# Kernel optimization log

Hardware: AMD Instinct MI355X
Metric: run time of the kernel (lower is better)

Reference implementation:

```python
import jax, jax.numpy as jnp
import numpy as np

B, S, DIN, DOUT = 2, 2048, 4096, 4096


def setup_inputs() -> dict:
    key = jax.random.key(0)
    k1, k2 = jax.random.split(key)
    x = jax.random.normal(k1, (B, S, DIN), dtype=jnp.float32)
    weight = jax.random.normal(k2, (DOUT, DIN), dtype=jnp.float32) * 0.02
    # xnor init for row scaling pattern
    mean = weight.mean(-1, keepdims=True)                      # [DOUT,1]
    scale = jnp.abs(weight - mean).mean(-1, keepdims=True)     # [DOUT,1]
    wscale = scale
    wbias = mean
    return {"x": x, "weight": weight, "wscale": wscale, "wbias": wbias}


def reference(x, weight, wscale, wbias):
    # STE binarization: forward = sign(weight) (grad handled in bwd module)
    w_bin = jnp.sign(weight)
    w = wscale * w_bin + wbias                                 # [DOUT, DIN]
    # F.linear(x, w): x @ w.T, no bias
    out = jnp.einsum('bsk,nk->bsn', x, w)
    return out
```

## Files before the change

kernel.cpp:

```cpp
#include <hip/hip_runtime.h>
#include <stdint.h>


#define MDIM 4096
#define NDIM 4096
#define KDIM 4096

typedef int int4v  __attribute__((ext_vector_type(4)));
typedef int int16v __attribute__((ext_vector_type(16)));

__device__ __forceinline__ int pack4_rn(float a, float b, float c, float d, float inv) {
  int ia = __float2int_rn(a * inv) & 0xff;
  int ib = __float2int_rn(b * inv) & 0xff;
  int ic = __float2int_rn(c * inv) & 0xff;
  int id = __float2int_rn(d * inv) & 0xff;
  return ia | (ib << 8) | (ic << 16) | (id << 24);
}

__device__ __forceinline__ int sgn8(float v) {
  return (v > 0.f) ? 1 : ((v < 0.f) ? 0xff : 0);
}

__global__ __launch_bounds__(256) void prep_kernel(
    const float* __restrict__ x, const float* __restrict__ w,
    char* __restrict__ xq, char* __restrict__ wsg,
    float* __restrict__ xscale, float* __restrict__ sumx) {
  const int b = blockIdx.x;
  const int tid = threadIdx.x;
  if (b < MDIM) {
    const int row = b;
    const float4* xr = (const float4*)(x + (size_t)row * KDIM);
    float4 v[4];
    float s = 0.f, amax = 0.f;
#pragma unroll
    for (int u = 0; u < 4; ++u) {
      v[u] = xr[u * 256 + tid];
      s += v[u].x + v[u].y + v[u].z + v[u].w;
      amax = fmaxf(amax, fmaxf(fmaxf(fabsf(v[u].x), fabsf(v[u].y)),
                               fmaxf(fabsf(v[u].z), fabsf(v[u].w))));
    }
#pragma unroll
    for (int off = 32; off > 0; off >>= 1) {
      s += __shfl_down(s, off, 64);
      amax = fmaxf(amax, __shfl_down(amax, off, 64));
    }
    __shared__ float rs[4], rm[4], bcast;
    if ((tid & 63) == 0) { rs[tid >> 6] = s; rm[tid >> 6] = amax; }
    __syncthreads();
    if (tid == 0) {
      sumx[row] = rs[0] + rs[1] + rs[2] + rs[3];
      float mt = fmaxf(fmaxf(rm[0], rm[1]), fmaxf(rm[2], rm[3]));
      xscale[row] = mt * (1.f / 127.f);
      bcast = (mt > 0.f) ? 127.f / mt : 0.f;
    }
    __syncthreads();
    const float inv = bcast;
    int* xo = (int*)(xq + (size_t)row * KDIM);
#pragma unroll
    for (int u = 0; u < 4; ++u)
      xo[u * 256 + tid] = pack4_rn(v[u].x, v[u].y, v[u].z, v[u].w, inv);
  } else {
    const size_t base = (size_t)(b - MDIM) * (256 * 4);
    const float4* wr = (const float4*)w;
    int* wo = (int*)wsg;
#pragma unroll
    for (int u = 0; u < 4; ++u) {
      size_t i = base + u * 256 + tid;
      float4 v = wr[i];
      wo[i] = sgn8(v.x) | (sgn8(v.y) << 8) | (sgn8(v.z) << 16) | (sgn8(v.w) << 24);
    }
  }
}

__global__ __launch_bounds__(512, 2) void gemm_bin_i8_pipe(
    const char* __restrict__ A, const char* __restrict__ Bs,
    const float* __restrict__ wscale, const float* __restrict__ wbias,
    const float* __restrict__ xscale, const float* __restrict__ sumx,
    float* __restrict__ C) {
  __shared__ __align__(16) char sm[131072];

  const int bm = blockIdx.x >> 4, bn = blockIdx.x & 15;
  const int tm0 = bm * 256, tn0 = bn * 256;
  const int tid = threadIdx.x;
  const int lane = tid & 63, wave = tid >> 6;
  const int col32 = lane & 31, hl = lane >> 5;
  const int wr = wave >> 2, wc = wave & 3;

  int16v acc[4][2];
#pragma unroll
  for (int mi = 0; mi < 4; ++mi)
#pragma unroll
    for (int nj = 0; nj < 2; ++nj)
#pragma unroll
      for (int r = 0; r < 16; ++r) acc[mi][nj][r] = 0;

  int4v afA[4], bqA[2], afB[4], bqB[2];

  int aOff[2][4], bOff[2][2];
#pragma unroll
  for (int ks2 = 0; ks2 < 2; ++ks2) {
#pragma unroll
    for (int mi = 0; mi < 4; ++mi) {
      int row = wr * 128 + mi * 32 + col32;
      int sw = (row >> 1) & 3;
      aOff[ks2][mi] = row * 64 + (((ks2 * 2 + hl) ^ sw) & 3) * 16;
    }
#pragma unroll
    for (int nj = 0; nj < 2; ++nj) {
      int row = wc * 64 + nj * 32 + col32;
      int sw = (row >> 1) & 3;
      bOff[ks2][nj] = 65536 + row * 64 + (((ks2 * 2 + hl) ^ sw) & 3) * 16;
    }
  }

  const int u0 = tid, u1 = tid + 512;
  const int r0 = u0 >> 2, r1 = u1 >> 2;
  const int c0 = (u0 & 3) ^ ((r0 >> 1) & 3);
  const int c1 = (u1 & 3) ^ ((r1 >> 1) & 3);
  const char* gA0 = A + (size_t)(tm0 + r0) * KDIM + c0 * 16;
  const char* gA1 = A + (size_t)(tm0 + r1) * KDIM + c1 * 16;
  const char* gB0 = Bs + (size_t)(tn0 + r0) * KDIM + c0 * 16;
  const char* gB1 = Bs + (size_t)(tn0 + r1) * KDIM + c1 * 16;
  const int ldsu0 = tid * 16, ldsu1 = 8192 + tid * 16;

#define STAGE_A(BUF, KH, KOFS)                                                    \
  do {                                                                            \
    const int base_ = ((BUF) * 2 + (KH)) * 16384;                                 \
    __builtin_amdgcn_global_load_lds(                                             \
        (const __attribute__((address_space(1))) void*)(gA0 + (KOFS)),            \
        (__attribute__((address_space(3))) void*)(sm + base_ + ldsu0), 16, 0, 0); \
    __builtin_amdgcn_global_load_lds(                                             \
        (const __attribute__((address_space(1))) void*)(gA1 + (KOFS)),            \
        (__attribute__((address_space(3))) void*)(sm + base_ + ldsu1), 16, 0, 0); \
  } while (0)

#define STAGE_B(BUF, KH, KOFS)                                                    \
  do {                                                                            \
    const int base_ = 65536 + ((BUF) * 2 + (KH)) * 16384;                         \
    __builtin_amdgcn_global_load_lds(                                             \
        (const __attribute__((address_space(1))) void*)(gB0 + (KOFS)),            \
        (__attribute__((address_space(3))) void*)(sm + base_ + ldsu0), 16, 0, 0); \
    __builtin_amdgcn_global_load_lds(                                             \
        (const __attribute__((address_space(1))) void*)(gB1 + (KOFS)),            \
        (__attribute__((address_space(3))) void*)(sm + base_ + ldsu1), 16, 0, 0); \
  } while (0)

#define DSRD(SET, BUF, KS, KS2)                                                   \
  do {                                                                            \
    _Pragma("unroll") for (int mi_ = 0; mi_ < 4; ++mi_)                           \
        af##SET[mi_] =                                                            \
            *(const int4v*)(sm + ((BUF) * 2 + (KS)) * 16384 + aOff[KS2][mi_]);    \
    _Pragma("unroll") for (int nj_ = 0; nj_ < 2; ++nj_)                           \
        bq##SET[nj_] =                                                            \
            *(const int4v*)(sm + ((BUF) * 2 + (KS)) * 16384 + bOff[KS2][nj_]);    \
  } while (0)

#define MFMA8(SET)                                                                \
  do {                                                                            \
    __builtin_amdgcn_s_setprio(1);                                                \
    _Pragma("unroll") for (int mi_ = 0; mi_ < 4; ++mi_)                           \
        _Pragma("unroll") for (int nj_ = 0; nj_ < 2; ++nj_)                       \
            acc[mi_][nj_] = __builtin_amdgcn_mfma_i32_32x32x32_i8(                \
                af##SET[mi_], bq##SET[nj_], acc[mi_][nj_], 0, 0, 0);              \
    __builtin_amdgcn_s_setprio(0);                                                \
  } while (0)

#define WAITL6                                                                    \
  do {                                                                            \
    asm volatile("s_waitcnt lgkmcnt(6)" ::: "memory");                            \
    __builtin_amdgcn_sched_barrier(0);                                            \
  } while (0)
#define WAITL0                                                                    \
  do {                                                                            \
    asm volatile("s_waitcnt lgkmcnt(0)" ::: "memory");                            \
    __builtin_amdgcn_sched_barrier(0);                                            \
  } while (0)

#define BARO __builtin_amdgcn_s_barrier()
#define CK6  asm volatile("s_waitcnt vmcnt(6)\n\ts_barrier" ::: "memory")
#define CK4  asm volatile("s_waitcnt vmcnt(4)\n\ts_barrier" ::: "memory")
#define CK0  asm volatile("s_waitcnt vmcnt(0)\n\ts_barrier" ::: "memory")

#define PHASEP(CSET, NSET, NBUF, NKS, NKS2, STAGEOP, ENDSYNC)                     \
  do {                                                                            \
    DSRD(NSET, NBUF, NKS, NKS2);                                                  \
    STAGEOP;                                                                      \
    WAITL6;                                                                       \
    MFMA8(CSET);                                                                  \
    ENDSYNC;                                                                      \
  } while (0)

#define TILE_MAIN(BUF, TAU)                                                       \
  do {                                                                            \
    PHASEP(A, B, BUF, 0, 1, STAGE_A((BUF) ^ 1, 1, ((TAU) + 1) * 128 + 64), BARO); \
    PHASEP(B, A, BUF, 1, 0, STAGE_B((BUF) ^ 1, 1, ((TAU) + 1) * 128 + 64), BARO); \
    PHASEP(A, B, BUF, 1, 1, STAGE_A(BUF, 0, ((TAU) + 2) * 128), CK6);             \
    PHASEP(B, A, (BUF) ^ 1, 0, 0, STAGE_B(BUF, 0, ((TAU) + 2) * 128), CK4);       \
  } while (0)

  STAGE_A(0, 0, 0);
  STAGE_B(0, 0, 0);
  STAGE_A(0, 1, 64);
  STAGE_B(0, 1, 64);
  STAGE_A(1, 0, 128);
  STAGE_B(1, 0, 128);
  CK4;
  DSRD(A, 0, 0, 0);

#pragma unroll 1
  for (int t = 0; t < 30; t += 2) {
    TILE_MAIN(0, t);
    TILE_MAIN(1, t + 1);
  }

  PHASEP(A, B, 0, 0, 1, STAGE_A(1, 1, 31 * 128 + 64), BARO);
  PHASEP(B, A, 0, 1, 0, STAGE_B(1, 1, 31 * 128 + 64), BARO);
  PHASEP(A, B, 0, 1, 1, (void)0, CK4);
  PHASEP(B, A, 1, 0, 0, (void)0, CK0);
  PHASEP(A, B, 1, 0, 1, (void)0, BARO);
  PHASEP(B, A, 1, 1, 0, (void)0, BARO);
  PHASEP(A, B, 1, 1, 1, (void)0, BARO);
  WAITL0;
  MFMA8(B);

#undef TILE_MAIN
#undef PHASEP
#undef BARO
#undef CK6
#undef CK4
#undef CK0
#undef WAITL6
#undef WAITL0
#undef MFMA8
#undef DSRD
#undef STAGE_A
#undef STAGE_B

  float wsv[2], wbv[2];
#pragma unroll
  for (int nj = 0; nj < 2; ++nj) {
    int n = tn0 + wc * 64 + nj * 32 + col32;
    wsv[nj] = wscale[n];
    wbv[nj] = wbias[n];
  }
#pragma unroll
  for (int mi = 0; mi < 4; ++mi) {
#pragma unroll
    for (int reg = 0; reg < 16; ++reg) {
      int m = tm0 + wr * 128 + mi * 32 + (reg & 3) + 8 * (reg >> 2) + 4 * hl;
      float xs = xscale[m];
      float sx = sumx[m];
      float* crow = C + (size_t)m * NDIM + tn0 + wc * 64 + col32;
#pragma unroll
      for (int nj = 0; nj < 2; ++nj)
        crow[nj * 32] = wsv[nj] * xs * (float)acc[mi][nj][reg] + wbv[nj] * sx;
    }
  }
}

extern "C" void kernel_launch(void* const* d_in, const int* in_sizes, int n_in,
                              void* d_out, int out_size, void* d_ws, size_t ws_size,
                              hipStream_t stream) {
  const float* x      = (const float*)d_in[0];
  const float* weight = (const float*)d_in[1];
  const float* wscale = (const float*)d_in[2];
  const float* wbias  = (const float*)d_in[3];
  float* out = (float*)d_out;

  char* xq  = (char*)d_ws;
  char* wsg = xq + (size_t)MDIM * KDIM;
  float* xscale = (float*)(wsg + (size_t)NDIM * KDIM);
  float* sumx   = xscale + MDIM;

  prep_kernel<<<MDIM + (NDIM * KDIM) / (16 * 256), 256, 0, stream>>>(
      x, weight, xq, wsg, xscale, sumx);
  gemm_bin_i8_pipe<<<(MDIM / 256) * (NDIM / 256), 512, 0, stream>>>(
      xq, wsg, wscale, wbias, xscale, sumx, out);
}
```

Measured before the change: 234.1 us.

## Use 4 waves per block with 128x128 per-wave tiles in int8 GEMM

Changes the GEMM block from 8 waves (each computing 128x64) to 4 waves, each computing 128x128 with 16 MFMAs per phase, keeping the 256x256 block tile and LDS layout. Each thread now issues 4 global-to-LDS loads per stage, so the vmcnt/lgkmcnt wait thresholds are raised to match. The intent is to cut LDS read traffic per MFMA and barrier overhead, at the cost of more accumulator registers (256 VGPRs of accumulators), fewer waves to hide latency, and one block per CU.

```diff
diff --git a/kernel.cpp b/kernel.cpp
--- a/kernel.cpp
+++ b/kernel.cpp
@@ -72,7 +72,7 @@
   }
 }
 
-__global__ __launch_bounds__(512, 2) void gemm_bin_i8_pipe(
+__global__ __launch_bounds__(256, 1) void gemm_bin_i8_w4(
     const char* __restrict__ A, const char* __restrict__ Bs,
     const float* __restrict__ wscale, const float* __restrict__ wbias,
     const float* __restrict__ xscale, const float* __restrict__ sumx,
@@ -84,19 +84,19 @@
   const int tid = threadIdx.x;
   const int lane = tid & 63, wave = tid >> 6;
   const int col32 = lane & 31, hl = lane >> 5;
-  const int wr = wave >> 2, wc = wave & 3;
-
-  int16v acc[4][2];
+  const int wr = wave >> 1, wc = wave & 1;
+
+  int16v acc[4][4];
 #pragma unroll
   for (int mi = 0; mi < 4; ++mi)
 #pragma unroll
-    for (int nj = 0; nj < 2; ++nj)
+    for (int nj = 0; nj < 4; ++nj)
 #pragma unroll
       for (int r = 0; r < 16; ++r) acc[mi][nj][r] = 0;
 
-  int4v afA[4], bqA[2], afB[4], bqB[2];
-
-  int aOff[2][4], bOff[2][2];
+  int4v afA[4], bqA[4], afB[4], bqB[4];
+
+  int aOff[2][4], bOff[2][4];
 #pragma unroll
   for (int ks2 = 0; ks2 < 2; ++ks2) {
 #pragma unroll
@@ -106,43 +106,43 @@
       aOff[ks2][mi] = row * 64 + (((ks2 * 2 + hl) ^ sw) & 3) * 16;
     }
 #pragma unroll
-    for (int nj = 0; nj < 2; ++nj) {
-      int row = wc * 64 + nj * 32 + col32;
+    for (int nj = 0; nj < 4; ++nj) {
+      int row = wc * 128 + nj * 32 + col32;
       int sw = (row >> 1) & 3;
       bOff[ks2][nj] = 65536 + row * 64 + (((ks2 * 2 + hl) ^ sw) & 3) * 16;
     }
   }
 
-  const int u0 = tid, u1 = tid + 512;
-  const int r0 = u0 >> 2, r1 = u1 >> 2;
-  const int c0 = (u0 & 3) ^ ((r0 >> 1) & 3);
-  const int c1 = (u1 & 3) ^ ((r1 >> 1) & 3);
-  const char* gA0 = A + (size_t)(tm0 + r0) * KDIM + c0 * 16;
-  const char* gA1 = A + (size_t)(tm0 + r1) * KDIM + c1 * 16;
-  const char* gB0 = Bs + (size_t)(tn0 + r0) * KDIM + c0 * 16;
-  const char* gB1 = Bs + (size_t)(tn0 + r1) * KDIM + c1 * 16;
-  const int ldsu0 = tid * 16, ldsu1 = 8192 + tid * 16;
+  const char* gAp[4];
+  const char* gBp[4];
+  int ldq[4];
+#pragma unroll
+  for (int q = 0; q < 4; ++q) {
+    int rowq = (tid >> 2) + 64 * q;
+    int cq = (tid & 3) ^ ((rowq >> 1) & 3);
+    gAp[q] = A + (size_t)(tm0 + rowq) * KDIM + cq * 16;
+    gBp[q] = Bs + (size_t)(tn0 + rowq) * KDIM + cq * 16;
+    ldq[q] = q * 4096 + tid * 16;
+  }
 
 #define STAGE_A(BUF, KH, KOFS)                                                    \
   do {                                                                            \
     const int base_ = ((BUF) * 2 + (KH)) * 16384;                                 \
-    __builtin_amdgcn_global_load_lds(                                             \
-        (const __attribute__((address_space(1))) void*)(gA0 + (KOFS)),            \
-        (__attribute__((address_space(3))) void*)(sm + base_ + ldsu0), 16, 0, 0); \
-    __builtin_amdgcn_global_load_lds(                                             \
-        (const __attribute__((address_space(1))) void*)(gA1 + (KOFS)),            \
-        (__attribute__((address_space(3))) void*)(sm + base_ + ldsu1), 16, 0, 0); \
+    _Pragma("unroll") for (int q_ = 0; q_ < 4; ++q_)                              \
+        __builtin_amdgcn_global_load_lds(                                         \
+            (const __attribute__((address_space(1))) void*)(gAp[q_] + (KOFS)),    \
+            (__attribute__((address_space(3))) void*)(sm + base_ + ldq[q_]),      \
+            16, 0, 0);                                                            \
   } while (0)
 
 #define STAGE_B(BUF, KH, KOFS)                                                    \
   do {                                                                            \
     const int base_ = 65536 + ((BUF) * 2 + (KH)) * 16384;                         \
-    __builtin_amdgcn_global_load_lds(                                             \
-        (const __attribute__((address_space(1))) void*)(gB0 + (KOFS)),            \
-        (__attribute__((address_space(3))) void*)(sm + base_ + ldsu0), 16, 0, 0); \
-    __builtin_amdgcn_global_load_lds(                                             \
-        (const __attribute__((address_space(1))) void*)(gB1 + (KOFS)),            \
-        (__attribute__((address_space(3))) void*)(sm + base_ + ldsu1), 16, 0, 0); \
+    _Pragma("unroll") for (int q_ = 0; q_ < 4; ++q_)                              \
+        __builtin_amdgcn_global_load_lds(                                         \
+            (const __attribute__((address_space(1))) void*)(gBp[q_] + (KOFS)),    \
+            (__attribute__((address_space(3))) void*)(sm + base_ + ldq[q_]),      \
+            16, 0, 0);                                                            \
   } while (0)
 
 #define DSRD(SET, BUF, KS, KS2)                                                   \
@@ -150,24 +150,24 @@
     _Pragma("unroll") for (int mi_ = 0; mi_ < 4; ++mi_)                           \
         af##SET[mi_] =                                                            \
             *(const int4v*)(sm + ((BUF) * 2 + (KS)) * 16384 + aOff[KS2][mi_]);    \
-    _Pragma("unroll") for (int nj_ = 0; nj_ < 2; ++nj_)                           \
+    _Pragma("unroll") for (int nj_ = 0; nj_ < 4; ++nj_)                           \
         bq##SET[nj_] =                                                            \
             *(const int4v*)(sm + ((BUF) * 2 + (KS)) * 16384 + bOff[KS2][nj_]);    \
   } while (0)
 
-#define MFMA8(SET)                                                                \
+#define MFMA16(SET)                                                               \
   do {                                                                            \
     __builtin_amdgcn_s_setprio(1);                                                \
     _Pragma("unroll") for (int mi_ = 0; mi_ < 4; ++mi_)                           \
-        _Pragma("unroll") for (int nj_ = 0; nj_ < 2; ++nj_)                       \
+        _Pragma("unroll") for (int nj_ = 0; nj_ < 4; ++nj_)                       \
             acc[mi_][nj_] = __builtin_amdgcn_mfma_i32_32x32x32_i8(                \
                 af##SET[mi_], bq##SET[nj_], acc[mi_][nj_], 0, 0, 0);              \
     __builtin_amdgcn_s_setprio(0);                                                \
   } while (0)
 
-#define WAITL6                                                                    \
-  do {                                                                            \
-    asm volatile("s_waitcnt lgkmcnt(6)" ::: "memory");                            \
+#define WAITL8                                                                    \
+  do {                                                                            \
+    asm volatile("s_waitcnt lgkmcnt(8)" ::: "memory");                            \
     __builtin_amdgcn_sched_barrier(0);                                            \
   } while (0)
 #define WAITL0                                                                    \
@@ -177,16 +177,16 @@
   } while (0)
 
 #define BARO __builtin_amdgcn_s_barrier()
-#define CK6  asm volatile("s_waitcnt vmcnt(6)\n\ts_barrier" ::: "memory")
-#define CK4  asm volatile("s_waitcnt vmcnt(4)\n\ts_barrier" ::: "memory")
+#define CK12 asm volatile("s_waitcnt vmcnt(12)\n\ts_barrier" ::: "memory")
+#define CK8  asm volatile("s_waitcnt vmcnt(8)\n\ts_barrier" ::: "memory")
 #define CK0  asm volatile("s_waitcnt vmcnt(0)\n\ts_barrier" ::: "memory")
 
 #define PHASEP(CSET, NSET, NBUF, NKS, NKS2, STAGEOP, ENDSYNC)                     \
   do {                                                                            \
     DSRD(NSET, NBUF, NKS, NKS2);                                                  \
     STAGEOP;                                                                      \
-    WAITL6;                                                                       \
-    MFMA8(CSET);                                                                  \
+    WAITL8;                                                                       \
+    MFMA16(CSET);                                                                 \
     ENDSYNC;                                                                      \
   } while (0)
 
@@ -194,8 +194,8 @@
   do {                                                                            \
     PHASEP(A, B, BUF, 0, 1, STAGE_A((BUF) ^ 1, 1, ((TAU) + 1) * 128 + 64), BARO); \
     PHASEP(B, A, BUF, 1, 0, STAGE_B((BUF) ^ 1, 1, ((TAU) + 1) * 128 + 64), BARO); \
-    PHASEP(A, B, BUF, 1, 1, STAGE_A(BUF, 0, ((TAU) + 2) * 128), CK6);             \
-    PHASEP(B, A, (BUF) ^ 1, 0, 0, STAGE_B(BUF, 0, ((TAU) + 2) * 128), CK4);       \
+    PHASEP(A, B, BUF, 1, 1, STAGE_A(BUF, 0, ((TAU) + 2) * 128), CK12);            \
+    PHASEP(B, A, (BUF) ^ 1, 0, 0, STAGE_B(BUF, 0, ((TAU) + 2) * 128), CK8);       \
   } while (0)
 
   STAGE_A(0, 0, 0);
@@ -204,7 +204,7 @@
   STAGE_B(0, 1, 64);
   STAGE_A(1, 0, 128);
   STAGE_B(1, 0, 128);
-  CK4;
+  CK8;
   DSRD(A, 0, 0, 0);
 
 #pragma unroll 1
@@ -215,31 +215,31 @@
 
   PHASEP(A, B, 0, 0, 1, STAGE_A(1, 1, 31 * 128 + 64), BARO);
   PHASEP(B, A, 0, 1, 0, STAGE_B(1, 1, 31 * 128 + 64), BARO);
-  PHASEP(A, B, 0, 1, 1, (void)0, CK4);
+  PHASEP(A, B, 0, 1, 1, (void)0, CK8);
   PHASEP(B, A, 1, 0, 0, (void)0, CK0);
   PHASEP(A, B, 1, 0, 1, (void)0, BARO);
   PHASEP(B, A, 1, 1, 0, (void)0, BARO);
   PHASEP(A, B, 1, 1, 1, (void)0, BARO);
   WAITL0;
-  MFMA8(B);
+  MFMA16(B);
 
 #undef TILE_MAIN
 #undef PHASEP
 #undef BARO
-#undef CK6
-#undef CK4
+#undef CK12
+#undef CK8
 #undef CK0
-#undef WAITL6
+#undef WAITL8
 #undef WAITL0
-#undef MFMA8
+#undef MFMA16
 #undef DSRD
 #undef STAGE_A
 #undef STAGE_B
 
-  float wsv[2], wbv[2];
-#pragma unroll
-  for (int nj = 0; nj < 2; ++nj) {
-    int n = tn0 + wc * 64 + nj * 32 + col32;
+  float wsv[4], wbv[4];
+#pragma unroll
+  for (int nj = 0; nj < 4; ++nj) {
+    int n = tn0 + wc * 128 + nj * 32 + col32;
     wsv[nj] = wscale[n];
     wbv[nj] = wbias[n];
   }
@@ -250,9 +250,9 @@
       int m = tm0 + wr * 128 + mi * 32 + (reg & 3) + 8 * (reg >> 2) + 4 * hl;
       float xs = xscale[m];
       float sx = sumx[m];
-      float* crow = C + (size_t)m * NDIM + tn0 + wc * 64 + col32;
-#pragma unroll
-      for (int nj = 0; nj < 2; ++nj)
+      float* crow = C + (size_t)m * NDIM + tn0 + wc * 128 + col32;
+#pragma unroll
+      for (int nj = 0; nj < 4; ++nj)
         crow[nj * 32] = wsv[nj] * xs * (float)acc[mi][nj][reg] + wbv[nj] * sx;
     }
   }
@@ -274,6 +274,6 @@
 
   prep_kernel<<<MDIM + (NDIM * KDIM) / (16 * 256), 256, 0, stream>>>(
       x, weight, xq, wsg, xscale, sumx);
-  gemm_bin_i8_pipe<<<(MDIM / 256) * (NDIM / 256), 512, 0, stream>>>(
+  gemm_bin_i8_w4<<<(MDIM / 256) * (NDIM / 256), 256, 0, stream>>>(
       xq, wsg, wscale, wbias, xscale, sumx, out);
 }
```

After: 233.0 us. No clear change (-0.5%).

## Shrink GEMM tile to 128x256 with 4 waves, K-step 32, XCD-aware block mapping

Applied to the files above, without the earlier changes.

The int8 binary GEMM now uses 128x256 block tiles with 256 threads (4 waves) instead of 256x256 with 512 threads. The K slice per stage drops from 64 to 32 bytes and LDS use falls from 128KB to 48KB, so several blocks can fit per CU. Block indices are remapped so that each XCD handles a contiguous 4x2 group of tiles, which is meant to improve L2 reuse. The grid doubles to 512 blocks to give better occupancy and wave balance. In exchange, each wave reloads more data per unit of MFMA work, and the smaller K steps mean twice as many barriers.

```diff
diff --git a/kernel.cpp b/kernel.cpp
--- a/kernel.cpp
+++ b/kernel.cpp
@@ -72,19 +72,22 @@
   }
 }
 
-__global__ __launch_bounds__(512, 2) void gemm_bin_i8_pipe(
+__global__ __launch_bounds__(256, 2) void gemm_bin_i8_2b(
     const char* __restrict__ A, const char* __restrict__ Bs,
     const float* __restrict__ wscale, const float* __restrict__ wbias,
     const float* __restrict__ xscale, const float* __restrict__ sumx,
     float* __restrict__ C) {
-  __shared__ __align__(16) char sm[131072];
-
-  const int bm = blockIdx.x >> 4, bn = blockIdx.x & 15;
-  const int tm0 = bm * 256, tn0 = bn * 256;
+  __shared__ __align__(16) char sm[49152];
+
+  const int bid = blockIdx.x;
+  const int xcd = bid & 7, loc = bid >> 3;
+  const int bm = (xcd >> 1) * 8 + (loc >> 3);
+  const int bn = (xcd & 1) * 8 + (loc & 7);
+  const int tm0 = bm * 128, tn0 = bn * 256;
   const int tid = threadIdx.x;
   const int lane = tid & 63, wave = tid >> 6;
   const int col32 = lane & 31, hl = lane >> 5;
-  const int wr = wave >> 2, wc = wave & 3;
+  const int wc = wave;
 
   int16v acc[4][2];
 #pragma unroll
@@ -96,63 +99,54 @@
 
   int4v afA[4], bqA[2], afB[4], bqB[2];
 
-  int aOff[2][4], bOff[2][2];
-#pragma unroll
-  for (int ks2 = 0; ks2 < 2; ++ks2) {
-#pragma unroll
-    for (int mi = 0; mi < 4; ++mi) {
-      int row = wr * 128 + mi * 32 + col32;
-      int sw = (row >> 1) & 3;
-      aOff[ks2][mi] = row * 64 + (((ks2 * 2 + hl) ^ sw) & 3) * 16;
-    }
-#pragma unroll
-    for (int nj = 0; nj < 2; ++nj) {
-      int row = wc * 64 + nj * 32 + col32;
-      int sw = (row >> 1) & 3;
-      bOff[ks2][nj] = 65536 + row * 64 + (((ks2 * 2 + hl) ^ sw) & 3) * 16;
-    }
-  }
-
-  const int u0 = tid, u1 = tid + 512;
-  const int r0 = u0 >> 2, r1 = u1 >> 2;
-  const int c0 = (u0 & 3) ^ ((r0 >> 1) & 3);
-  const int c1 = (u1 & 3) ^ ((r1 >> 1) & 3);
-  const char* gA0 = A + (size_t)(tm0 + r0) * KDIM + c0 * 16;
-  const char* gA1 = A + (size_t)(tm0 + r1) * KDIM + c1 * 16;
-  const char* gB0 = Bs + (size_t)(tn0 + r0) * KDIM + c0 * 16;
-  const char* gB1 = Bs + (size_t)(tn0 + r1) * KDIM + c1 * 16;
-  const int ldsu0 = tid * 16, ldsu1 = 8192 + tid * 16;
-
-#define STAGE_A(BUF, KH, KOFS)                                                    \
-  do {                                                                            \
-    const int base_ = ((BUF) * 2 + (KH)) * 16384;                                 \
+  int aOff[4], bOff[2];
+#pragma unroll
+  for (int mi = 0; mi < 4; ++mi) {
+    int row = mi * 32 + col32;
+    aOff[mi] = row * 32 + ((hl ^ ((row >> 2) & 1)) & 1) * 16;
+  }
+#pragma unroll
+  for (int nj = 0; nj < 2; ++nj) {
+    int row = wc * 64 + nj * 32 + col32;
+    bOff[nj] = row * 32 + ((hl ^ ((row >> 2) & 1)) & 1) * 16;
+  }
+
+  const int rA = tid >> 1;
+  const int cA = (tid & 1) ^ ((rA >> 2) & 1);
+  const char* gA0 = A + (size_t)(tm0 + rA) * KDIM + cA * 16;
+  const char* gBp[2];
+#pragma unroll
+  for (int q = 0; q < 2; ++q) {
+    int u = tid + 256 * q;
+    int row = u >> 1;
+    int c = (u & 1) ^ ((row >> 2) & 1);
+    gBp[q] = Bs + (size_t)(tn0 + row) * KDIM + c * 16;
+  }
+  const int ldA = tid * 16, ldB0 = tid * 16, ldB1 = 4096 + tid * 16;
+
+#define STAGE3(BUF, KH, KOFS)                                                     \
+  do {                                                                            \
+    const int baseA_ = ((BUF) * 2 + (KH)) * 4096;                                 \
+    const int baseB_ = 16384 + ((BUF) * 2 + (KH)) * 8192;                         \
     __builtin_amdgcn_global_load_lds(                                             \
         (const __attribute__((address_space(1))) void*)(gA0 + (KOFS)),            \
-        (__attribute__((address_space(3))) void*)(sm + base_ + ldsu0), 16, 0, 0); \
+        (__attribute__((address_space(3))) void*)(sm + baseA_ + ldA), 16, 0, 0);  \
     __builtin_amdgcn_global_load_lds(                                             \
-        (const __attribute__((address_space(1))) void*)(gA1 + (KOFS)),            \
-        (__attribute__((address_space(3))) void*)(sm + base_ + ldsu1), 16, 0, 0); \
-  } while (0)
-
-#define STAGE_B(BUF, KH, KOFS)                                                    \
-  do {                                                                            \
-    const int base_ = 65536 + ((BUF) * 2 + (KH)) * 16384;                         \
+        (const __attribute__((address_space(1))) void*)(gBp[0] + (KOFS)),         \
+        (__attribute__((address_space(3))) void*)(sm + baseB_ + ldB0), 16, 0, 0); \
     __builtin_amdgcn_global_load_lds(                                             \
-        (const __attribute__((address_space(1))) void*)(gB0 + (KOFS)),            \
-        (__attribute__((address_space(3))) void*)(sm + base_ + ldsu0), 16, 0, 0); \
-    __builtin_amdgcn_global_load_lds(                                             \
-        (const __attribute__((address_space(1))) void*)(gB1 + (KOFS)),            \
-        (__attribute__((address_space(3))) void*)(sm + base_ + ldsu1), 16, 0, 0); \
-  } while (0)
-
-#define DSRD(SET, BUF, KS, KS2)                                                   \
-  do {                                                                            \
+        (const __attribute__((address_space(1))) void*)(gBp[1] + (KOFS)),         \
+        (__attribute__((address_space(3))) void*)(sm + baseB_ + ldB1), 16, 0, 0); \
+  } while (0)
+
+#define DSRD(SET, BUF, KS)                                                        \
+  do {                                                                            \
+    const int baseA_ = ((BUF) * 2 + (KS)) * 4096;                                 \
+    const int baseB_ = 16384 + ((BUF) * 2 + (KS)) * 8192;                         \
     _Pragma("unroll") for (int mi_ = 0; mi_ < 4; ++mi_)                           \
-        af##SET[mi_] =                                                            \
-            *(const int4v*)(sm + ((BUF) * 2 + (KS)) * 16384 + aOff[KS2][mi_]);    \
+        af##SET[mi_] = *(const int4v*)(sm + baseA_ + aOff[mi_]);                  \
     _Pragma("unroll") for (int nj_ = 0; nj_ < 2; ++nj_)                           \
-        bq##SET[nj_] =                                                            \
-            *(const int4v*)(sm + ((BUF) * 2 + (KS)) * 16384 + bOff[KS2][nj_]);    \
+        bq##SET[nj_] = *(const int4v*)(sm + baseB_ + bOff[nj_]);                  \
   } while (0)
 
 #define MFMA8(SET)                                                                \
@@ -176,14 +170,12 @@
     __builtin_amdgcn_sched_barrier(0);                                            \
   } while (0)
 
-#define BARO __builtin_amdgcn_s_barrier()
-#define CK6  asm volatile("s_waitcnt vmcnt(6)\n\ts_barrier" ::: "memory")
-#define CK4  asm volatile("s_waitcnt vmcnt(4)\n\ts_barrier" ::: "memory")
-#define CK0  asm volatile("s_waitcnt vmcnt(0)\n\ts_barrier" ::: "memory")
-
-#define PHASEP(CSET, NSET, NBUF, NKS, NKS2, STAGEOP, ENDSYNC)                     \
-  do {                                                                            \
-    DSRD(NSET, NBUF, NKS, NKS2);                                                  \
+#define CKV3 asm volatile("s_waitcnt vmcnt(3)\n\ts_barrier" ::: "memory")
+#define CKV0 asm volatile("s_waitcnt vmcnt(0)\n\ts_barrier" ::: "memory")
+
+#define PHASEP(CSET, NSET, NBUF, NKS, STAGEOP, ENDSYNC)                           \
+  do {                                                                            \
+    DSRD(NSET, NBUF, NKS);                                                        \
     STAGEOP;                                                                      \
     WAITL6;                                                                       \
     MFMA8(CSET);                                                                  \
@@ -192,49 +184,37 @@
 
 #define TILE_MAIN(BUF, TAU)                                                       \
   do {                                                                            \
-    PHASEP(A, B, BUF, 0, 1, STAGE_A((BUF) ^ 1, 1, ((TAU) + 1) * 128 + 64), BARO); \
-    PHASEP(B, A, BUF, 1, 0, STAGE_B((BUF) ^ 1, 1, ((TAU) + 1) * 128 + 64), BARO); \
-    PHASEP(A, B, BUF, 1, 1, STAGE_A(BUF, 0, ((TAU) + 2) * 128), CK6);             \
-    PHASEP(B, A, (BUF) ^ 1, 0, 0, STAGE_B(BUF, 0, ((TAU) + 2) * 128), CK4);       \
-  } while (0)
-
-  STAGE_A(0, 0, 0);
-  STAGE_B(0, 0, 0);
-  STAGE_A(0, 1, 64);
-  STAGE_B(0, 1, 64);
-  STAGE_A(1, 0, 128);
-  STAGE_B(1, 0, 128);
-  CK4;
-  DSRD(A, 0, 0, 0);
+    PHASEP(A, B, BUF, 1, STAGE3((BUF) ^ 1, 1, ((TAU) + 1) * 64 + 32), CKV3);      \
+    PHASEP(B, A, (BUF) ^ 1, 0, STAGE3(BUF, 0, ((TAU) + 2) * 64), CKV3);           \
+  } while (0)
+
+  STAGE3(0, 0, 0);
+  STAGE3(0, 1, 32);
+  STAGE3(1, 0, 64);
+  CKV3;
+  DSRD(A, 0, 0);
 
 #pragma unroll 1
-  for (int t = 0; t < 30; t += 2) {
+  for (int t = 0; t < 62; t += 2) {
     TILE_MAIN(0, t);
     TILE_MAIN(1, t + 1);
   }
 
-  PHASEP(A, B, 0, 0, 1, STAGE_A(1, 1, 31 * 128 + 64), BARO);
-  PHASEP(B, A, 0, 1, 0, STAGE_B(1, 1, 31 * 128 + 64), BARO);
-  PHASEP(A, B, 0, 1, 1, (void)0, CK4);
-  PHASEP(B, A, 1, 0, 0, (void)0, CK0);
-  PHASEP(A, B, 1, 0, 1, (void)0, BARO);
-  PHASEP(B, A, 1, 1, 0, (void)0, BARO);
-  PHASEP(A, B, 1, 1, 1, (void)0, BARO);
+  PHASEP(A, B, 0, 1, STAGE3(1, 1, 63 * 64 + 32), CKV3);
+  PHASEP(B, A, 1, 0, (void)0, CKV0);
+  PHASEP(A, B, 1, 1, (void)0, (void)0);
   WAITL0;
   MFMA8(B);
 
 #undef TILE_MAIN
 #undef PHASEP
-#undef BARO
-#undef CK6
-#undef CK4
-#undef CK0
+#undef CKV3
+#undef CKV0
 #undef WAITL6
 #undef WAITL0
 #undef MFMA8
 #undef DSRD
-#undef STAGE_A
-#undef STAGE_B
+#undef STAGE3
 
   float wsv[2], wbv[2];
 #pragma unroll
@@ -247,7 +227,7 @@
   for (int mi = 0; mi < 4; ++mi) {
 #pragma unroll
     for (int reg = 0; reg < 16; ++reg) {
-      int m = tm0 + wr * 128 + mi * 32 + (reg & 3) + 8 * (reg >> 2) + 4 * hl;
+      int m = tm0 + mi * 32 + (reg & 3) + 8 * (reg >> 2) + 4 * hl;
       float xs = xscale[m];
       float sx = sumx[m];
       float* crow = C + (size_t)m * NDIM + tn0 + wc * 64 + col32;
@@ -274,6 +254,6 @@
 
   prep_kernel<<<MDIM + (NDIM * KDIM) / (16 * 256), 256, 0, stream>>>(
       x, weight, xq, wsg, xscale, sumx);
-  gemm_bin_i8_pipe<<<(MDIM / 256) * (NDIM / 256), 512, 0, stream>>>(
+  gemm_bin_i8_2b<<<(MDIM / 128) * (NDIM / 256), 256, 0, stream>>>(
       xq, wsg, wscale, wbias, xscale, sumx, out);
 }
```

Measured after the change: 271.6 us. 1.16x slower.
